# Kernel optimization log

Measured on AMD Instinct MI355X. Metric: run time of the kernel, lower is better.

Reference implementation:

```python
import jax, jax.numpy as jnp
import numpy as np

N_NODES = 100000


def gcn_conv(x, W, b, src, dst, n):
    # PyG GCNConv: linear transform, add self-loops, symmetric deg^-1/2 norm,
    # scatter-sum messages from src -> dst, add bias.
    x = x @ W  # [N, out]
    loop = jnp.arange(n, dtype=src.dtype)
    src_sl = jnp.concatenate([src, loop])
    dst_sl = jnp.concatenate([dst, loop])
    deg = jax.ops.segment_sum(jnp.ones_like(dst_sl, dtype=x.dtype), dst_sl, num_segments=n)
    dinv = jax.lax.rsqrt(deg)
    norm = dinv[src_sl] * dinv[dst_sl]  # [E+N]
    msg = x[src_sl] * norm[:, None]
    out = jax.ops.segment_sum(msg, dst_sl, num_segments=n)
    return out + b


def base_gnn(x, edge_index, W1, b1, W2, b2):
    src, dst = edge_index[0], edge_index[1]
    n = x.shape[0]
    h = gcn_conv(x, W1, b1, src, dst, n)
    h = jax.nn.relu(h)
    return gcn_conv(h, W2, b2, src, dst, n)


def setup_inputs() -> dict:
    key = jax.random.key(0)
    ks = jax.random.split(key, 12)
    n, e, ep, en = N_NODES, 1600000, 200000, 200000
    in_ch, hid, out_ch, n_classes = 256, 128, 128, 10
    x = jax.random.normal(ks[0], (n, in_ch), dtype=jnp.float32)
    edge_index = jax.random.randint(ks[1], (2, e), 0, n, dtype=jnp.int64)
    edge_index_pos = jax.random.randint(ks[2], (2, ep), 0, n, dtype=jnp.int64)
    edge_index_neg = jax.random.randint(ks[3], (2, en), 0, n, dtype=jnp.int64)
    s1 = 1.0 / np.sqrt(in_ch)
    s2 = 1.0 / np.sqrt(hid)
    so = 1.0 / np.sqrt(out_ch)
    sl = 1.0 / np.sqrt(2 * out_ch)
    return {
        "x": x,
        "edge_index": edge_index,
        "edge_index_pos": edge_index_pos,
        "edge_index_neg": edge_index_neg,
        "W1": jax.random.uniform(ks[4], (in_ch, hid), jnp.float32, -s1, s1),
        "b1": jnp.zeros((hid,), jnp.float32),
        "W2": jax.random.uniform(ks[5], (hid, out_ch), jnp.float32, -s2, s2),
        "b2": jnp.zeros((out_ch,), jnp.float32),
        "Wcls": jax.random.uniform(ks[6], (out_ch, n_classes), jnp.float32, -so, so),
        "bcls": jax.random.uniform(ks[7], (n_classes,), jnp.float32, -so, so),
        "Wlink": jax.random.uniform(ks[8], (2 * out_ch, 1), jnp.float32, -sl, sl),
        "blink": jax.random.uniform(ks[9], (1,), jnp.float32, -sl, sl),
    }


def reference(x, edge_index, edge_index_pos, edge_index_neg,
              W1, b1, W2, b2, Wcls, bcls, Wlink, blink):
    # Shared base embedding (math identical to torch's redundant recompute)
    h = base_gnn(x, edge_index, W1, b1, W2, b2)  # [N, 128]
    # Node head
    node_logits = jax.nn.relu(h) @ Wcls + bcls
    node_pred = jax.nn.log_softmax(node_logits, axis=1)
    # Link head: gather endpoint embeddings, concat, linear
    xp = jnp.concatenate([h[edge_index_pos[0]], h[edge_index_pos[1]]], axis=1)
    xn = jnp.concatenate([h[edge_index_neg[0]], h[edge_index_neg[1]]], axis=1)
    link_pos = (xp @ Wlink + blink)[:, 0]
    link_neg = (xn @ Wlink + blink)[:, 0]
    return (node_pred, link_pos, link_neg)
```

## Files before the change

kernel.cpp:

```cpp
#include <hip/hip_runtime.h>
#include <stdint.h>

typedef __attribute__((ext_vector_type(8))) short bf16x8;
typedef __attribute__((ext_vector_type(4))) float f32x4;

__device__ __forceinline__ float b2f(uint32_t h) {
    union { uint32_t u; float f; } v; v.u = h << 16; return v.f;
}
__device__ __forceinline__ ushort f2b(float f) {
    union { float f; uint32_t u; } v; v.f = f;
    uint32_t u = v.u;
    return (ushort)((u + 0x7fffu + ((u >> 16) & 1u)) >> 16);
}
__device__ __forceinline__ float ldin(const void* p, int i, int fp32) {
    return fp32 ? ((const float*)p)[i] : b2f(((const ushort*)p)[i]);
}

__device__ __forceinline__ void sniff(const void* W1, const void* ei, int* sf) {
    if (threadIdx.x < 64) {
        int l = threadIdx.x;
        const ushort* w = (const ushort*)W1;
        bool bad = !(fabsf(b2f(w[l])) <= 0.25f) || !(fabsf(b2f(w[64 + l])) <= 0.25f);
        unsigned long long mb = __ballot(bad);
        const int* e = (const int*)ei;
        bool z = (l < 16) ? (e[2 * l + 1] == 0) : false;
        unsigned long long mz = __ballot(z);
        if (l == 0) {
            sf[0] = mb ? 1 : 0;
            sf[1] = (__popcll(mz & 0xffffull) >= 15) ? 1 : 0;
        }
    }
    __syncthreads();
}


__global__ __launch_bounds__(256) void k_prep(const void* __restrict__ x,
                                              const void* ei, const void* ep, const void* en,
                                              const void* W1, const void* b1, const void* W2,
                                              const void* b2, const void* Wc, const void* bc,
                                              const void* Wl, const void* bl,
                                              int* cEi, int* cEp, int* cEn,
                                              ushort* __restrict__ xc,
                                              ushort* Wt1, ushort* Wt2, ushort* WtC,
                                              ushort* b1c, ushort* b2c, ushort* bcc,
                                              ushort* Wlc, ushort* blc,
                                              int* __restrict__ histM,
                                              int twoE, int twoEp, int twoEn, int N,
                                              int E, int NB1,
                                              int Bidx, int Bw, int Bx) {
    __shared__ int sf[2];
    __shared__ int h[512];
    sniff(W1, ei, sf);
    int f = sf[0], i64 = sf[1];
    int b = blockIdx.x;

    if (b < Bidx) {
        int i = (b * 256 + threadIdx.x) * 2;
        const void* srcp; int* dstp; int j = i;
        if (i < twoE) { srcp = ei; dstp = cEi; }
        else if (i < twoE + twoEp) { srcp = ep; dstp = cEp; j = i - twoE; }
        else if (i < twoE + twoEp + twoEn) { srcp = en; dstp = cEn; j = i - twoE - twoEp; }
        else return;
        int v0, v1;
        if (i64) {
            longlong2 t = *(const longlong2*)((const long long*)srcp + j);
            v0 = (int)t.x; v1 = (int)t.y;
        } else {
            int2 t = *(const int2*)((const int*)srcp + j);
            v0 = t.x; v1 = t.y;
        }
        v0 = v0 < 0 ? 0 : (v0 >= N ? N - 1 : v0);
        v1 = v1 < 0 ? 0 : (v1 >= N ? N - 1 : v1);
        *(int2*)(dstp + j) = make_int2(v0, v1);
    } else if (b < Bidx + Bw) {
        int i = (b - Bidx) * 256 + threadIdx.x;
        if (i < 32768) {
            int c = i >> 8, kpos = i & 255;
            int s = kpos >> 5, t = kpos & 31, q = t >> 3, jj = t & 7;
            int k = s * 32 + (jj < 4 ? q * 4 + jj : 16 + q * 4 + (jj - 4));
            Wt1[i] = f2b(ldin(W1, k * 128 + c, f));
        } else if (i < 49152) {
            int j = i - 32768, c = j >> 7, k = j & 127;
            Wt2[j] = f2b(ldin(W2, k * 128 + c, f));
        } else if (i < 51200) {
            int j = i - 49152, c = j >> 7, k = j & 127;
            ushort v = 0;
            if (c < 10) v = f2b(ldin(Wc, k * 10 + c, f));
            WtC[j] = v;
        } else if (i < 51328) {
            int j = i - 51200; b1c[j] = f2b(ldin(b1, j, f));
        } else if (i < 51456) {
            int j = i - 51328; b2c[j] = f2b(ldin(b2, j, f));
        } else if (i < 51472) {
            int j = i - 51456;
            ushort v = 0;
            if (j < 10) v = f2b(ldin(bc, j, f));
            bcc[j] = v;
        } else if (i < 51728) {
            int j = i - 51472; Wlc[j] = f2b(ldin(Wl, j, f));
        } else if (i < 51736) {
            int j = i - 51728;
            ushort v = 0;
            if (j < 1) v = f2b(ldin(bl, 0, f));
            blc[j] = v;
        }
    } else if (b < Bidx + Bw + Bx) {
        int gw = (b - Bidx - Bw) * 4 + (threadIdx.x >> 6);
        int ntile = (N + 15) >> 4;
        if (gw >= ntile * 4) return;
        int tile = gw >> 2, s2 = gw & 3;
        int l = threadIdx.x & 63, mr = l & 15, q = l >> 4;
        int row = tile * 16 + mr;
        if (row > N - 1) row = N - 1;
#pragma unroll
        for (int u = 0; u < 2; ++u) {
            int s = s2 * 2 + u;
            uint4 o;
            if (f) {
                const float* xf = (const float*)x + (size_t)row * 256 + s * 32;
                float4 a = *(const float4*)(xf + q * 4);
                float4 bb = *(const float4*)(xf + 16 + q * 4);
                o.x = (uint32_t)f2b(a.x) | ((uint32_t)f2b(a.y) << 16);
                o.y = (uint32_t)f2b(a.z) | ((uint32_t)f2b(a.w) << 16);
                o.z = (uint32_t)f2b(bb.x) | ((uint32_t)f2b(bb.y) << 16);
                o.w = (uint32_t)f2b(bb.z) | ((uint32_t)f2b(bb.w) << 16);
            } else {
                const ushort* xs = (const ushort*)x + (size_t)row * 256 + s * 32;
                uint2 lo = *(const uint2*)(xs + q * 4);
                uint2 hi = *(const uint2*)(xs + 16 + q * 4);
                o.x = lo.x; o.y = lo.y; o.z = hi.x; o.w = hi.y;
            }
            *(uint4*)(xc + ((size_t)(tile * 8 + s) * 64 + l) * 8) = o;
        }
    } else {
        int b2 = b - Bidx - Bw - Bx;
        for (int j = threadIdx.x; j < 512; j += 256) h[j] = 0;
        __syncthreads();
        int base = b2 * 4096;
        for (int j = threadIdx.x; j < 4096; j += 256) {
            int i = base + j;
            if (i < E) {
                int d = i64 ? (int)((const long long*)ei)[E + i] : ((const int*)ei)[E + i];
                d = d < 0 ? 0 : (d >= N ? N - 1 : d);
                atomicAdd(&h[d >> 8], 1);
            }
        }
        __syncthreads();
        for (int j = threadIdx.x; j < 512; j += 256)
            histM[j * NB1 + b2] = h[j];
    }
}

__global__ __launch_bounds__(1024) void k_mscan_block(const int* __restrict__ in, int* __restrict__ out,
                                                      int* __restrict__ bsum, int len) {
    __shared__ int sh[1024];
    int t = threadIdx.x;
    int i = blockIdx.x * 1024 + t;
    int val = (i < len) ? in[i] : 0;
    sh[t] = val; __syncthreads();
    for (int off = 1; off < 1024; off <<= 1) {
        int v = (t >= off) ? sh[t - off] : 0;
        __syncthreads();
        sh[t] += v;
        __syncthreads();
    }
    if (i < len) out[i] = sh[t] - val;
    if (t == 1023) bsum[blockIdx.x] = sh[1023];
}

__global__ __launch_bounds__(1024) void k_mscan_topadd(int* __restrict__ out, const int* __restrict__ bsum,
                                                       int* __restrict__ cbs, int len, int mb,
                                                       int NB1, int E) {
    __shared__ int sh[1024];
    int t = threadIdx.x;
    sh[t] = (t < mb) ? bsum[t] : 0; __syncthreads();
    for (int off = 1; off < 1024; off <<= 1) {
        int v = (t >= off) ? sh[t - off] : 0;
        __syncthreads();
        sh[t] += v;
        __syncthreads();
    }
    int pref = (blockIdx.x > 0) ? sh[blockIdx.x - 1] : 0;
    int i = blockIdx.x * 1024 + t;
    if (i < len) {
        int v = out[i] + pref;
        out[i] = v;
        if (i % NB1 == 0) cbs[i / NB1] = v;
    }
    if (i == 0) cbs[512] = E;
}

__global__ __launch_bounds__(256) void k_scatter1(const int* __restrict__ src, const int* __restrict__ dst,
                                                  const int* __restrict__ off, int2* __restrict__ grouped,
                                                  int E, int NB1) {
    __shared__ int o[512];
    for (int j = threadIdx.x; j < 512; j += 256) o[j] = off[j * NB1 + blockIdx.x];
    __syncthreads();
    int base = blockIdx.x * 4096;
    for (int j = threadIdx.x; j < 4096; j += 256) {
        int i = base + j;
        if (i < E) {
            int d = dst[i];
            int p = atomicAdd(&o[d >> 8], 1);
            grouped[p] = make_int2(src[i], d);
        }
    }
}

__global__ __launch_bounds__(256) void k_degscan(const int2* __restrict__ grouped, const int* __restrict__ cbs,
                                                 int* __restrict__ rowptr, float* __restrict__ dinv,
                                                 int N, int E) {
    __shared__ int cnt[256];
    int t = threadIdx.x, b = blockIdx.x;
    cnt[t] = 0;
    __syncthreads();
    int s0 = cbs[b], s1 = cbs[b + 1];
    for (int i = s0 + t; i < s1; i += 256)
        atomicAdd(&cnt[grouped[i].y & 255], 1);
    __syncthreads();
    int deg = cnt[t];
    __syncthreads();
    for (int off = 1; off < 256; off <<= 1) {
        int vv = (t >= off) ? cnt[t - off] : 0;
        __syncthreads();
        cnt[t] += vv;
        __syncthreads();
    }
    int excl = cnt[t] - deg;
    int v = b * 256 + t;
    if (v < N) {
        rowptr[v] = s0 + excl;
        dinv[v] = rsqrtf((float)(deg + 1));
    }
    if (b == 0 && t == 0) rowptr[N] = E;
}

__global__ __launch_bounds__(256) void k_fill2(const int2* __restrict__ grouped, const int* __restrict__ cbs,
                                               const int* __restrict__ rowptr, const float* __restrict__ dinv,
                                               int2* __restrict__ edge, int N) {
    __shared__ int o[256];
    int b = blockIdx.x;
    int v = b * 256 + threadIdx.x;
    o[threadIdx.x] = (v < N) ? rowptr[v] : 0;
    __syncthreads();
    int s0 = cbs[b], s1 = cbs[b + 1];
    for (int i = s0 + threadIdx.x; i < s1; i += 256) {
        int2 e = grouped[i];
        int p = atomicAdd(&o[e.y & 255], 1);
        float w = dinv[e.x] * dinv[e.y];
        edge[p] = make_int2(e.x, __float_as_int(w));
    }
}

template <int NS>
__global__ __launch_bounds__(256) void k_gemm(const ushort* __restrict__ Xf,
                                              const ushort* __restrict__ Wt,
                                              ushort* __restrict__ Out, int nrows) {
    __shared__ uint4 sB[NS * 8 * 64];

    const int tid = threadIdx.x;
    for (int it = tid; it < NS * 8 * 64; it += 256) {
        int l = it & 63, fn = it >> 6;
        int s = fn >> 3, n = fn & 7;
        int mr = l & 15, q = l >> 4;
        sB[it] = *(const uint4*)(Wt + (size_t)(n * 16 + mr) * (NS * 32) + s * 32 + q * 8);
    }
    __syncthreads();

    const int wave = tid >> 6;
    const int l = tid & 63;
    const int q = l >> 4, mr = l & 15;
    const int gw = blockIdx.x * 4 + wave;
    const int nw = gridDim.x * 4;
    const int ntile = (nrows + 15) >> 4;

    for (int tp = gw; tp * 4 < ntile; tp += nw) {
        const int t0 = tp * 4;
        const bool h1 = (t0 + 1 < ntile), h2 = (t0 + 2 < ntile), h3 = (t0 + 3 < ntile);
        const int tb1 = h1 ? t0 + 1 : t0, tb2 = h2 ? t0 + 2 : t0, tb3 = h3 ? t0 + 3 : t0;

        const ushort* x0 = Xf + ((size_t)t0 * NS * 64 + l) * 8;
        const ushort* x1 = Xf + ((size_t)tb1 * NS * 64 + l) * 8;
        const ushort* x2 = Xf + ((size_t)tb2 * NS * 64 + l) * 8;
        const ushort* x3 = Xf + ((size_t)tb3 * NS * 64 + l) * 8;

        f32x4 accA[8], accB[8], accC[8], accD[8];
#pragma unroll
        for (int n = 0; n < 8; ++n) {
            accA[n] = (f32x4){0.f, 0.f, 0.f, 0.f};
            accB[n] = (f32x4){0.f, 0.f, 0.f, 0.f};
            accC[n] = (f32x4){0.f, 0.f, 0.f, 0.f};
            accD[n] = (f32x4){0.f, 0.f, 0.f, 0.f};
        }
#pragma unroll
        for (int s = 0; s < NS; ++s) {
            bf16x8 a0 = *(const bf16x8*)(x0 + s * 512);
            bf16x8 a1 = *(const bf16x8*)(x1 + s * 512);
            bf16x8 a2 = *(const bf16x8*)(x2 + s * 512);
            bf16x8 a3 = *(const bf16x8*)(x3 + s * 512);
#pragma unroll
            for (int n = 0; n < 8; ++n) {
                bf16x8 bfr = __builtin_bit_cast(bf16x8, sB[(s * 8 + n) * 64 + l]);
                accA[n] = __builtin_amdgcn_mfma_f32_16x16x32_bf16(bfr, a0, accA[n], 0, 0, 0);
                accB[n] = __builtin_amdgcn_mfma_f32_16x16x32_bf16(bfr, a1, accB[n], 0, 0, 0);
                accC[n] = __builtin_amdgcn_mfma_f32_16x16x32_bf16(bfr, a2, accC[n], 0, 0, 0);
                accD[n] = __builtin_amdgcn_mfma_f32_16x16x32_bf16(bfr, a3, accD[n], 0, 0, 0);
            }
        }
        {
            int row = t0 * 16 + mr;
            if (row < nrows) {
                ushort* orow = Out + (size_t)row * 128 + q * 4;
#pragma unroll
                for (int n = 0; n < 8; ++n) {
                    uint2 o;
                    o.x = (uint32_t)f2b(accA[n][0]) | ((uint32_t)f2b(accA[n][1]) << 16);
                    o.y = (uint32_t)f2b(accA[n][2]) | ((uint32_t)f2b(accA[n][3]) << 16);
                    *(uint2*)(orow + n * 16) = o;
                }
            }
        }
        if (h1) {
            int row = tb1 * 16 + mr;
            if (row < nrows) {
                ushort* orow = Out + (size_t)row * 128 + q * 4;
#pragma unroll
                for (int n = 0; n < 8; ++n) {
                    uint2 o;
                    o.x = (uint32_t)f2b(accB[n][0]) | ((uint32_t)f2b(accB[n][1]) << 16);
                    o.y = (uint32_t)f2b(accB[n][2]) | ((uint32_t)f2b(accB[n][3]) << 16);
                    *(uint2*)(orow + n * 16) = o;
                }
            }
        }
        if (h2) {
            int row = tb2 * 16 + mr;
            if (row < nrows) {
                ushort* orow = Out + (size_t)row * 128 + q * 4;
#pragma unroll
                for (int n = 0; n < 8; ++n) {
                    uint2 o;
                    o.x = (uint32_t)f2b(accC[n][0]) | ((uint32_t)f2b(accC[n][1]) << 16);
                    o.y = (uint32_t)f2b(accC[n][2]) | ((uint32_t)f2b(accC[n][3]) << 16);
                    *(uint2*)(orow + n * 16) = o;
                }
            }
        }
        if (h3) {
            int row = tb3 * 16 + mr;
            if (row < nrows) {
                ushort* orow = Out + (size_t)row * 128 + q * 4;
#pragma unroll
                for (int n = 0; n < 8; ++n) {
                    uint2 o;
                    o.x = (uint32_t)f2b(accD[n][0]) | ((uint32_t)f2b(accD[n][1]) << 16);
                    o.y = (uint32_t)f2b(accD[n][2]) | ((uint32_t)f2b(accD[n][3]) << 16);
                    *(uint2*)(orow + n * 16) = o;
                }
            }
        }
    }
}

__device__ __forceinline__ void fma8(float* acc, uint4 p, float w) {
    uint32_t pu[4] = {p.x, p.y, p.z, p.w};
#pragma unroll
    for (int k = 0; k < 4; ++k) {
        float lo = __uint_as_float(pu[k] << 16);
        float hi = __uint_as_float(pu[k] & 0xffff0000u);
        acc[2 * k]     += lo * w;
        acc[2 * k + 1] += hi * w;
    }
}

__global__ __launch_bounds__(256) void k_conv(const ushort* __restrict__ XW, const int* __restrict__ rowptr,
                                              const int2* __restrict__ edge, const float* __restrict__ dinv,
                                              const ushort* __restrict__ bias, ushort* __restrict__ Hout,
                                              int n, int relu, int frag) {
    int wave = threadIdx.x >> 6;
    int v = blockIdx.x * 4 + wave;
    if (v >= n) return;
    int l = threadIdx.x & 63;
    int g = l >> 4;
    int c = l & 15;

    int s0 = rowptr[v], s1 = rowptr[v + 1];
    float dv = dinv[v];
    float wself = (g == 0) ? dv * dv : 0.f;

    uint4 pv = *(const uint4*)(XW + (size_t)v * 128 + c * 8);
    float acc[8];
    {
        uint32_t pu[4] = {pv.x, pv.y, pv.z, pv.w};
#pragma unroll
        for (int k = 0; k < 4; ++k) {
            acc[2 * k]     = __uint_as_float(pu[k] << 16) * wself;
            acc[2 * k + 1] = __uint_as_float(pu[k] & 0xffff0000u) * wself;
        }
    }

    int i = s0;
    while (i + 8 <= s1) {
        int2 eA = edge[i + g];
        int2 eB = edge[i + 4 + g];
        uint4 pA = *(const uint4*)(XW + (size_t)eA.x * 128 + c * 8);
        uint4 pB = *(const uint4*)(XW + (size_t)eB.x * 128 + c * 8);
        fma8(acc, pA, __int_as_float(eA.y));
        fma8(acc, pB, __int_as_float(eB.y));
        i += 8;
    }
    if (i + 4 <= s1) {
        int2 e = edge[i + g];
        uint4 p = *(const uint4*)(XW + (size_t)e.x * 128 + c * 8);
        fma8(acc, p, __int_as_float(e.y));
        i += 4;
    }
    if (i < s1) {
        int ei = i + g;
        bool val = ei < s1;
        int2 e = edge[val ? ei : s0];
        uint4 p = *(const uint4*)(XW + (size_t)e.x * 128 + c * 8);
        fma8(acc, p, val ? __int_as_float(e.y) : 0.f);
    }

#pragma unroll
    for (int k = 0; k < 8; ++k) {
        acc[k] += __shfl_xor(acc[k], 16);
        acc[k] += __shfl_xor(acc[k], 32);
    }

    if (g == 0) {
        uint4 bb = *(const uint4*)(bias + c * 8);
        uint32_t bu[4] = {bb.x, bb.y, bb.z, bb.w};
        uint4 o;
        uint32_t* op = (uint32_t*)&o;
#pragma unroll
        for (int k = 0; k < 4; ++k) {
            float lo = acc[2 * k]     + __uint_as_float(bu[k] << 16);
            float hi = acc[2 * k + 1] + __uint_as_float(bu[k] & 0xffff0000u);
            if (relu) { lo = fmaxf(lo, 0.f); hi = fmaxf(hi, 0.f); }
            op[k] = (uint32_t)f2b(lo) | ((uint32_t)f2b(hi) << 16);
        }
        if (frag) {
            int tile = v >> 4, mr = v & 15;
            size_t chunk = ((size_t)(tile * 4 + (c >> 2)) * 64 + (c & 3) * 16 + mr);
            *(uint4*)(Hout + chunk * 8) = o;
        } else {
            *(uint4*)(Hout + (size_t)v * 128 + c * 8) = o;
        }
    }
}

__global__ __launch_bounds__(256) void k_nodehead(const ushort* __restrict__ H, const ushort* __restrict__ WtC,
                                                  const ushort* __restrict__ bcc, const ushort* __restrict__ Wlc,
                                                  float2* __restrict__ ab, void* __restrict__ out,
                                                  int n, const void* W1s, const void* eis) {
    __shared__ int sf[2];
    sniff(W1s, eis, sf);
    int fp32o = sf[0];
    int wave = threadIdx.x >> 6;
    int gw = blockIdx.x * 4 + wave;
    if (gw * 16 >= n) return;
    int l = threadIdx.x & 63;
    int q = l >> 4, mr = l & 15;
    int m0 = gw * 16;

    const ushort* hrow = H + (size_t)(m0 + mr) * 128 + q * 8;
    bf16x8 araw[4];
#pragma unroll
    for (int s = 0; s < 4; ++s) araw[s] = *(const bf16x8*)(hrow + s * 32);

    float pa = 0.f, pb = 0.f;
#pragma unroll
    for (int s = 0; s < 4; ++s) {
        bf16x8 w0 = *(const bf16x8*)(Wlc + s * 32 + q * 8);
        bf16x8 w1 = *(const bf16x8*)(Wlc + 128 + s * 32 + q * 8);
#pragma unroll
        for (int j = 0; j < 8; ++j) {
            float hv = b2f((ushort)araw[s][j]);
            pa += hv * b2f((ushort)w0[j]);
            pb += hv * b2f((ushort)w1[j]);
        }
    }
    pa += __shfl_xor(pa, 16); pa += __shfl_xor(pa, 32);
    pb += __shfl_xor(pb, 16); pb += __shfl_xor(pb, 32);
    if (q == 0 && (m0 + mr) < n) ab[m0 + mr] = make_float2(pa, pb);

    f32x4 acc = (f32x4){0.f, 0.f, 0.f, 0.f};
#pragma unroll
    for (int s = 0; s < 4; ++s) {
        bf16x8 a = araw[s];
#pragma unroll
        for (int j = 0; j < 8; ++j) {
            ushort t = (ushort)a[j];
            if (t & 0x8000u) a[j] = 0;
        }
        bf16x8 b = *(const bf16x8*)(WtC + (size_t)mr * 128 + s * 32 + q * 8);
        acc = __builtin_amdgcn_mfma_f32_16x16x32_bf16(a, b, acc, 0, 0, 0);
    }

    float bc = b2f(bcc[mr]);
#pragma unroll
    for (int r = 0; r < 4; ++r) {
        float logit = acc[r] + bc;
        float m = (mr < 10) ? logit : -1e30f;
#pragma unroll
        for (int off = 1; off < 16; off <<= 1) m = fmaxf(m, __shfl_xor(m, off, 16));
        float ex = (mr < 10) ? expf(logit - m) : 0.f;
        float ssum = ex;
#pragma unroll
        for (int off = 1; off < 16; off <<= 1) ssum += __shfl_xor(ssum, off, 16);
        int row = m0 + q * 4 + r;
        if (mr < 10 && row < n) {
            float lsm = logit - m - logf(ssum);
            size_t idx = (size_t)row * 10 + mr;
            if (fp32o) ((float*)out)[idx] = lsm;
            else ((ushort*)out)[idx] = f2b(lsm);
        }
    }
}

__global__ __launch_bounds__(256) void k_linkfast(const float2* __restrict__ ab, const int* __restrict__ pos,
                                                  const int* __restrict__ neg, const ushort* __restrict__ blc,
                                                  void* __restrict__ out, size_t obase, int Ep, int En,
                                                  const void* W1s, const void* eis) {
    __shared__ int sf[2];
    sniff(W1s, eis, sf);
    int i = blockIdx.x * 256 + threadIdx.x;
    if (i >= Ep + En) return;
    int s, d;
    if (i < Ep) { s = pos[i]; d = pos[Ep + i]; }
    else { int j = i - Ep; s = neg[j]; d = neg[En + j]; }
    float vf = ab[s].x + ab[d].y + b2f(blc[0]);
    size_t idx = obase + (size_t)i;
    if (sf[0]) ((float*)out)[idx] = vf;
    else ((ushort*)out)[idx] = f2b(vf);
}

extern "C" void kernel_launch(void* const* d_in, const int* in_sizes, int n_in,
                              void* d_out, int out_size, void* d_ws, size_t ws_size,
                              hipStream_t stream) {
    const void* x    = d_in[0];
    const void* ei   = d_in[1];
    const void* eip  = d_in[2];
    const void* ein  = d_in[3];
    const void* W1   = d_in[4];
    const void* b1   = d_in[5];
    const void* W2   = d_in[6];
    const void* b2   = d_in[7];
    const void* Wcls = d_in[8];
    const void* bcls = d_in[9];
    const void* Wl   = d_in[10];
    const void* bl   = d_in[11];

    const int N  = in_sizes[0] / 256;
    const int E  = in_sizes[1] / 2;
    const int Ep = in_sizes[2] / 2;
    const int En = in_sizes[3] / 2;

    const int NB1  = (E + 4095) / 4096;
    const int mlen = 512 * NB1;
    const int mb   = (mlen + 1023) / 1024;
    const int ntile = (N + 15) / 16;

    char* ws = (char*)d_ws;
    size_t off = 0;
    auto alloc = [&](size_t bytes) -> void* {
        void* p = ws + off;
        off = (off + bytes + 255) & ~(size_t)255;
        return p;
    };
    ushort* xc     = (ushort*)alloc((size_t)ntile * 8 * 64 * 16);
    ushort* bufXW  = (ushort*)alloc((size_t)N * 128 * 2);
    ushort* bufH   = (ushort*)alloc((size_t)ntile * 4 * 64 * 16);
    float2* ab     = (float2*)alloc((size_t)N * 8);
    int*    cEi    = (int*)alloc((size_t)2 * E * 4);
    int*    cEp    = (int*)alloc((size_t)2 * Ep * 4);
    int*    cEn    = (int*)alloc((size_t)2 * En * 4);
    int2*   grouped= (int2*)alloc((size_t)E * 8);
    int*    histM  = (int*)alloc((size_t)mlen * 4);
    int*    offM   = (int*)alloc((size_t)mlen * 4);
    int*    msum   = (int*)alloc(4096);
    int*    cbs    = (int*)alloc(513 * 4);
    float*  dinv   = (float*)alloc((size_t)N * 4);
    int*    rowp   = (int*)alloc((size_t)(N + 1) * 4);
    int2*   edge   = (int2*)alloc((size_t)E * 8);
    ushort* Wt1    = (ushort*)alloc(65536);
    ushort* Wt2    = (ushort*)alloc(32768);
    ushort* WtC    = (ushort*)alloc(4096);
    ushort* b1c    = (ushort*)alloc(256);
    ushort* b2c    = (ushort*)alloc(256);
    ushort* bcc    = (ushort*)alloc(64);
    ushort* Wlc    = (ushort*)alloc(512);
    ushort* blc    = (ushort*)alloc(64);

    int twoE = 2 * E, twoEp = 2 * Ep, twoEn = 2 * En;
    int idx_total = twoE + twoEp + twoEn;
    int Bidx = (idx_total + 511) / 512;
    int Bw   = 203;
    int Bx   = ntile;

    k_prep<<<Bidx + Bw + Bx + NB1, 256, 0, stream>>>(x, ei, eip, ein, W1, b1, W2, b2, Wcls, bcls, Wl, bl,
                                                     cEi, cEp, cEn, xc, Wt1, Wt2, WtC,
                                                     b1c, b2c, bcc, Wlc, blc, histM,
                                                     twoE, twoEp, twoEn, N, E, NB1,
                                                     Bidx, Bw, Bx);

    const int* srcp = cEi;
    const int* dstp = cEi + E;

    k_mscan_block<<<mb, 1024, 0, stream>>>(histM, offM, msum, mlen);
    k_mscan_topadd<<<mb, 1024, 0, stream>>>(offM, msum, cbs, mlen, mb, NB1, E);
    k_scatter1<<<NB1, 256, 0, stream>>>(srcp, dstp, offM, grouped, E, NB1);
    k_degscan<<<512, 256, 0, stream>>>(grouped, cbs, rowp, dinv, N, E);
    k_fill2<<<512, 256, 0, stream>>>(grouped, cbs, rowp, dinv, edge, N);

    int quads = (ntile + 3) / 4;
    int g1 = (quads + 3) / 4; if (g1 > 768) g1 = 768;
    k_gemm<8><<<g1, 256, 0, stream>>>(xc, Wt1, bufXW, N);
    k_conv<<<(N + 3) / 4, 256, 0, stream>>>(bufXW, rowp, edge, dinv, b1c, bufH, N, 1, 1);
    k_gemm<4><<<g1, 256, 0, stream>>>(bufH, Wt2, bufXW, N);
    k_conv<<<(N + 3) / 4, 256, 0, stream>>>(bufXW, rowp, edge, dinv, b2c, bufH, N, 0, 0);

    int head_blocks = ((N + 15) / 16 + 3) / 4;
    k_nodehead<<<head_blocks, 256, 0, stream>>>(bufH, WtC, bcc, Wlc, ab, d_out, N, W1, ei);
    k_linkfast<<<(Ep + En + 255) / 256, 256, 0, stream>>>(ab, cEp, cEn, blc, d_out,
                                                          (size_t)N * 10, Ep, En, W1, ei);
}
```

Baseline: 453.8 us.

## Fuse degree scan with CSR fill and store source-only edge indices

```diff
diff --git a/kernel.cpp b/kernel.cpp
--- a/kernel.cpp
+++ b/kernel.cpp
@@ -45,7 +45,7 @@
                                               ushort* b1c, ushort* b2c, ushort* bcc,
                                               ushort* Wlc, ushort* blc,
                                               int* __restrict__ histM,
-                                              int twoE, int twoEp, int twoEn, int N,
+                                              int twoEp, int twoEn, int N,
                                               int E, int NB1,
                                               int Bidx, int Bw, int Bx) {
     __shared__ int sf[2];
@@ -57,9 +57,9 @@
     if (b < Bidx) {
         int i = (b * 256 + threadIdx.x) * 2;
         const void* srcp; int* dstp; int j = i;
-        if (i < twoE) { srcp = ei; dstp = cEi; }
-        else if (i < twoE + twoEp) { srcp = ep; dstp = cEp; j = i - twoE; }
-        else if (i < twoE + twoEp + twoEn) { srcp = en; dstp = cEn; j = i - twoE - twoEp; }
+        if (i < E) { srcp = ei; dstp = cEi; }
+        else if (i < E + twoEp) { srcp = ep; dstp = cEp; j = i - E; }
+        else if (i < E + twoEp + twoEn) { srcp = en; dstp = cEn; j = i - E - twoEp; }
         else return;
         int v0, v1;
         if (i64) {
@@ -142,6 +142,7 @@
             if (i < E) {
                 int d = i64 ? (int)((const long long*)ei)[E + i] : ((const int*)ei)[E + i];
                 d = d < 0 ? 0 : (d >= N ? N - 1 : d);
+                cEi[E + i] = d;
                 atomicAdd(&h[d >> 8], 1);
             }
         }
@@ -207,10 +208,11 @@
     }
 }
 
-__global__ __launch_bounds__(256) void k_degscan(const int2* __restrict__ grouped, const int* __restrict__ cbs,
+__global__ __launch_bounds__(256) void k_degfill(const int2* __restrict__ grouped, const int* __restrict__ cbs,
                                                  int* __restrict__ rowptr, float* __restrict__ dinv,
-                                                 int N, int E) {
+                                                 int* __restrict__ edgeS, int N, int E) {
     __shared__ int cnt[256];
+    __shared__ int obase[256];
     int t = threadIdx.x, b = blockIdx.x;
     cnt[t] = 0;
     __syncthreads();
@@ -233,22 +235,12 @@
         dinv[v] = rsqrtf((float)(deg + 1));
     }
     if (b == 0 && t == 0) rowptr[N] = E;
-}
-
-__global__ __launch_bounds__(256) void k_fill2(const int2* __restrict__ grouped, const int* __restrict__ cbs,
-                                               const int* __restrict__ rowptr, const float* __restrict__ dinv,
-                                               int2* __restrict__ edge, int N) {
-    __shared__ int o[256];
-    int b = blockIdx.x;
-    int v = b * 256 + threadIdx.x;
-    o[threadIdx.x] = (v < N) ? rowptr[v] : 0;
+    obase[t] = s0 + excl;
     __syncthreads();
-    int s0 = cbs[b], s1 = cbs[b + 1];
-    for (int i = s0 + threadIdx.x; i < s1; i += 256) {
+    for (int i = s0 + t; i < s1; i += 256) {
         int2 e = grouped[i];
-        int p = atomicAdd(&o[e.y & 255], 1);
-        float w = dinv[e.x] * dinv[e.y];
-        edge[p] = make_int2(e.x, __float_as_int(w));
+        int p = atomicAdd(&obase[e.y & 255], 1);
+        edgeS[p] = e.x;
     }
 }
 
@@ -374,7 +366,7 @@
 }
 
 __global__ __launch_bounds__(256) void k_conv(const ushort* __restrict__ XW, const int* __restrict__ rowptr,
-                                              const int2* __restrict__ edge, const float* __restrict__ dinv,
+                                              const int* __restrict__ edgeS, const float* __restrict__ dinv,
                                               const ushort* __restrict__ bias, ushort* __restrict__ Hout,
                                               int n, int relu, int frag) {
     int wave = threadIdx.x >> 6;
@@ -400,27 +392,45 @@
     }
 
     int i = s0;
-    while (i + 8 <= s1) {
-        int2 eA = edge[i + g];
-        int2 eB = edge[i + 4 + g];
-        uint4 pA = *(const uint4*)(XW + (size_t)eA.x * 128 + c * 8);
-        uint4 pB = *(const uint4*)(XW + (size_t)eB.x * 128 + c * 8);
-        fma8(acc, pA, __int_as_float(eA.y));
-        fma8(acc, pB, __int_as_float(eB.y));
+    while (i + 16 <= s1) {
+        int sA = edgeS[i + g];
+        int sB = edgeS[i + 4 + g];
+        int sC = edgeS[i + 8 + g];
+        int sD = edgeS[i + 12 + g];
+        uint4 pA = *(const uint4*)(XW + (size_t)sA * 128 + c * 8);
+        uint4 pB = *(const uint4*)(XW + (size_t)sB * 128 + c * 8);
+        uint4 pC = *(const uint4*)(XW + (size_t)sC * 128 + c * 8);
+        uint4 pD = *(const uint4*)(XW + (size_t)sD * 128 + c * 8);
+        float wA = dinv[sA] * dv, wB = dinv[sB] * dv;
+        float wC = dinv[sC] * dv, wD = dinv[sD] * dv;
+        fma8(acc, pA, wA);
+        fma8(acc, pB, wB);
+        fma8(acc, pC, wC);
+        fma8(acc, pD, wD);
+        i += 16;
+    }
+    if (i + 8 <= s1) {
+        int sA = edgeS[i + g];
+        int sB = edgeS[i + 4 + g];
+        uint4 pA = *(const uint4*)(XW + (size_t)sA * 128 + c * 8);
+        uint4 pB = *(const uint4*)(XW + (size_t)sB * 128 + c * 8);
+        float wA = dinv[sA] * dv, wB = dinv[sB] * dv;
+        fma8(acc, pA, wA);
+        fma8(acc, pB, wB);
         i += 8;
     }
     if (i + 4 <= s1) {
-        int2 e = edge[i + g];
-        uint4 p = *(const uint4*)(XW + (size_t)e.x * 128 + c * 8);
-        fma8(acc, p, __int_as_float(e.y));
+        int sA = edgeS[i + g];
+        uint4 pA = *(const uint4*)(XW + (size_t)sA * 128 + c * 8);
+        fma8(acc, pA, dinv[sA] * dv);
         i += 4;
     }
     if (i < s1) {
-        int ei = i + g;
-        bool val = ei < s1;
-        int2 e = edge[val ? ei : s0];
-        uint4 p = *(const uint4*)(XW + (size_t)e.x * 128 + c * 8);
-        fma8(acc, p, val ? __int_as_float(e.y) : 0.f);
+        int ei_ = i + g;
+        bool val = ei_ < s1;
+        int sA = edgeS[val ? ei_ : s0];
+        uint4 pA = *(const uint4*)(XW + (size_t)sA * 128 + c * 8);
+        fma8(acc, pA, val ? dinv[sA] * dv : 0.f);
     }
 
 #pragma unroll
@@ -584,7 +594,7 @@
     int*    cbs    = (int*)alloc(513 * 4);
     float*  dinv   = (float*)alloc((size_t)N * 4);
     int*    rowp   = (int*)alloc((size_t)(N + 1) * 4);
-    int2*   edge   = (int2*)alloc((size_t)E * 8);
+    int*    edgeS  = (int*)alloc((size_t)E * 4);
     ushort* Wt1    = (ushort*)alloc(65536);
     ushort* Wt2    = (ushort*)alloc(32768);
     ushort* WtC    = (ushort*)alloc(4096);
@@ -594,8 +604,8 @@
     ushort* Wlc    = (ushort*)alloc(512);
     ushort* blc    = (ushort*)alloc(64);
 
-    int twoE = 2 * E, twoEp = 2 * Ep, twoEn = 2 * En;
-    int idx_total = twoE + twoEp + twoEn;
+    int twoEp = 2 * Ep, twoEn = 2 * En;
+    int idx_total = E + twoEp + twoEn;
     int Bidx = (idx_total + 511) / 512;
     int Bw   = 203;
     int Bx   = ntile;
@@ -603,7 +613,7 @@
     k_prep<<<Bidx + Bw + Bx + NB1, 256, 0, stream>>>(x, ei, eip, ein, W1, b1, W2, b2, Wcls, bcls, Wl, bl,
                                                      cEi, cEp, cEn, xc, Wt1, Wt2, WtC,
                                                      b1c, b2c, bcc, Wlc, blc, histM,
-                                                     twoE, twoEp, twoEn, N, E, NB1,
+                                                     twoEp, twoEn, N, E, NB1,
                                                      Bidx, Bw, Bx);
 
     const int* srcp = cEi;
@@ -612,15 +622,14 @@
     k_mscan_block<<<mb, 1024, 0, stream>>>(histM, offM, msum, mlen);
     k_mscan_topadd<<<mb, 1024, 0, stream>>>(offM, msum, cbs, mlen, mb, NB1, E);
     k_scatter1<<<NB1, 256, 0, stream>>>(srcp, dstp, offM, grouped, E, NB1);
-    k_degscan<<<512, 256, 0, stream>>>(grouped, cbs, rowp, dinv, N, E);
-    k_fill2<<<512, 256, 0, stream>>>(grouped, cbs, rowp, dinv, edge, N);
+    k_degfill<<<512, 256, 0, stream>>>(grouped, cbs, rowp, dinv, edgeS, N, E);
 
     int quads = (ntile + 3) / 4;
     int g1 = (quads + 3) / 4; if (g1 > 768) g1 = 768;
     k_gemm<8><<<g1, 256, 0, stream>>>(xc, Wt1, bufXW, N);
-    k_conv<<<(N + 3) / 4, 256, 0, stream>>>(bufXW, rowp, edge, dinv, b1c, bufH, N, 1, 1);
+    k_conv<<<(N + 3) / 4, 256, 0, stream>>>(bufXW, rowp, edgeS, dinv, b1c, bufH, N, 1, 1);
     k_gemm<4><<<g1, 256, 0, stream>>>(bufH, Wt2, bufXW, N);
-    k_conv<<<(N + 3) / 4, 256, 0, stream>>>(bufXW, rowp, edge, dinv, b2c, bufH, N, 0, 0);
+    k_conv<<<(N + 3) / 4, 256, 0, stream>>>(bufXW, rowp, edgeS, dinv, b2c, bufH, N, 0, 0);
 
     int head_blocks = ((N + 15) / 16 + 3) / 4;
     k_nodehead<<<head_blocks, 256, 0, stream>>>(bufH, WtC, bcc, Wlc, ab, d_out, N, W1, ei);
```

Result: faster. 444.7 us (-2.0%).
